# Kernel optimization log

Hardware: AMD Instinct MI355X
Metric: run time of the kernel (lower is better)

## Reference

```python
import jax, jax.numpy as jnp
import numpy as np

N_NODES = 50000
N_EDGES = 800000
DIM_IN, DIM_H, DIM_OUT = 128, 128, 64


def _init_linear(key, fan_in, fan_out):
    # kaiming-uniform-ish init, matches torch Linear scale
    lim = 1.0 / np.sqrt(fan_in)
    return jax.random.uniform(key, (fan_in, fan_out), jnp.float32, -lim, lim)


def setup_inputs() -> dict:
    key = jax.random.key(0)
    ks = jax.random.split(key, 12)
    x = jax.random.normal(ks[0], (N_NODES, DIM_IN), jnp.float32)
    edge_index = jax.random.randint(ks[1], (2, N_EDGES), 0, N_NODES, jnp.int32)
    dims = [(DIM_IN, DIM_H), (DIM_H, DIM_H), (DIM_H, DIM_OUT)]
    inp = {"x": x, "edge_index": edge_index}
    for i, (fi, fo) in enumerate(dims):
        inp[f"Wl{i}"] = _init_linear(ks[2 + 3 * i], fi, fo)   # neighbor transform
        inp[f"Wr{i}"] = _init_linear(ks[3 + 3 * i], fi, fo)   # root transform
        inp[f"b{i}"] = jnp.zeros((fo,), jnp.float32)
    return inp


def _sage_layer(x, src, dst, Wl, Wr, b):
    # mean aggregation of neighbor messages x[src] at destination nodes
    msg = x[src]                                              # [E, d]
    agg = jax.ops.segment_sum(msg, dst, num_segments=N_NODES)  # [N, d]
    cnt = jax.ops.segment_sum(jnp.ones((src.shape[0],), x.dtype), dst,
                              num_segments=N_NODES)
    mean = agg / jnp.maximum(cnt, 1.0)[:, None]               # isolated nodes -> 0
    return mean @ Wl + b + x @ Wr                              # SAGEConv


def reference(x, edge_index, Wl0, Wr0, b0, Wl1, Wr1, b1, Wl2, Wr2, b2):
    src, dst = edge_index[0], edge_index[1]
    layers = [(Wl0, Wr0, b0), (Wl1, Wr1, b1), (Wl2, Wr2, b2)]
    h = x
    for i, (Wl, Wr, b) in enumerate(layers):
        h = _sage_layer(h, src, dst, Wl, Wr, b)
        if i != len(layers) - 1:
            h = jax.nn.relu(h)  # dropout p=0.2 is identity in eval mode
    return jax.nn.log_softmax(h, axis=1), h
```

## Files before the change

kernel.cpp:

```cpp
#include <hip/hip_runtime.h>

#define N_NODES 50000
#define N_EDGES 800000
#define SCAN_BLOCKS 196
#define WIN 6250

typedef __attribute__((ext_vector_type(8))) short short8;
typedef __attribute__((ext_vector_type(4))) float f32x4;
typedef unsigned short ushort_t;
typedef unsigned int uint_t;

__device__ inline ushort_t f2bf(float f) {
    union { float f; uint_t u; } v; v.f = f;
    uint_t u = v.u;
    u += 0x7fffu + ((u >> 16) & 1u);
    return (ushort_t)(u >> 16);
}
__device__ inline float bflo(uint_t v) { return __uint_as_float(v << 16); }
__device__ inline float bfhi(uint_t v) { return __uint_as_float(v & 0xffff0000u); }
__device__ inline float bf2f(ushort_t v) { return __uint_as_float((uint_t)v << 16); }

#define ACC8(V) { a[0] += bflo((V).x); a[1] += bfhi((V).x); \
                  a[2] += bflo((V).y); a[3] += bfhi((V).y); \
                  a[4] += bflo((V).z); a[5] += bfhi((V).z); \
                  a[6] += bflo((V).w); a[7] += bfhi((V).w); }

__global__ void count_edges_mp(const int* __restrict__ ei, int* __restrict__ cnt) {
    int g = blockIdx.x & 7;
    int nb = gridDim.x >> 3;
    int bi = blockIdx.x >> 3;
    int lo = g * WIN;
    for (int e = bi * 256 + threadIdx.x; e < N_EDGES; e += nb * 256) {
        int d = ei[N_EDGES + e];
        if ((unsigned)(d - lo) < WIN) atomicAdd(&cnt[d], 1);
    }
}

__global__ void fill_csr_mp(const int* __restrict__ ei, int* __restrict__ cursor,
                            int* __restrict__ csr_src) {
    int g = blockIdx.x & 7;
    int nb = gridDim.x >> 3;
    int bi = blockIdx.x >> 3;
    int lo = g * WIN;
    for (int e = bi * 256 + threadIdx.x; e < N_EDGES; e += nb * 256) {
        int d = ei[N_EDGES + e];
        if ((unsigned)(d - lo) < WIN) {
            int p = atomicAdd(&cursor[d], 1);
            csr_src[p] = ei[e];
        }
    }
}

__global__ void block_sums(const int* __restrict__ cnt, int* __restrict__ bsum) {
    int i = blockIdx.x * 256 + threadIdx.x;
    int v = (i < N_NODES) ? cnt[i] : 0;
    for (int off = 32; off; off >>= 1) v += __shfl_down(v, off, 64);
    __shared__ int s[4];
    if ((threadIdx.x & 63) == 0) s[threadIdx.x >> 6] = v;
    __syncthreads();
    if (threadIdx.x == 0) bsum[blockIdx.x] = s[0] + s[1] + s[2] + s[3];
}

__global__ void scan_bsums(const int* __restrict__ bsum, int* __restrict__ bprefix,
                           int* __restrict__ rowstart) {
    __shared__ int s[256];
    int t = threadIdx.x;
    int v = (t < SCAN_BLOCKS) ? bsum[t] : 0;
    s[t] = v;
    __syncthreads();
    for (int off = 1; off < 256; off <<= 1) {
        int add = (t >= off) ? s[t - off] : 0;
        __syncthreads();
        s[t] += add;
        __syncthreads();
    }
    bprefix[t] = s[t] - v;
    if (t == 0) rowstart[N_NODES] = N_EDGES;
}

__global__ void apply_scan(const int* __restrict__ cnt, const int* __restrict__ bprefix,
                           int* __restrict__ rowstart, int* __restrict__ cursor) {
    __shared__ int s[256];
    int t = threadIdx.x;
    int i = blockIdx.x * 256 + t;
    int v = (i < N_NODES) ? cnt[i] : 0;
    s[t] = v;
    __syncthreads();
    for (int off = 1; off < 256; off <<= 1) {
        int add = (t >= off) ? s[t - off] : 0;
        __syncthreads();
        s[t] += add;
        __syncthreads();
    }
    int excl = s[t] - v + bprefix[blockIdx.x];
    if (i < N_NODES) { rowstart[i] = excl; cursor[i] = excl; }
}

__global__ void cvt_bf16(const float* __restrict__ in, ushort_t* __restrict__ out, int n4) {
    int i = blockIdx.x * 256 + threadIdx.x;
    if (i < n4) {
        float4 v = ((const float4*)in)[i];
        ushort4 o;
        o.x = f2bf(v.x); o.y = f2bf(v.y); o.z = f2bf(v.z); o.w = f2bf(v.w);
        ((ushort4*)out)[i] = o;
    }
}

__global__ void pack_w256(const float* __restrict__ Wl, const float* __restrict__ Wr,
                          ushort_t* __restrict__ out) {
    int idx = blockIdx.x * 256 + threadIdx.x;
    if (idx >= 8 * 8 * 64 * 8) return;
    int j = idx & 7, l = (idx >> 3) & 63, t = (idx >> 9) & 7, ks = idx >> 12;
    int n = t * 16 + (l & 15);
    int k = ks * 32 + (l >> 4) * 8 + j;
    float w = (k < 128) ? Wl[k * 128 + n] : Wr[(k - 128) * 128 + n];
    out[idx] = f2bf(w);
}

__global__ void pack_wzr(const float* __restrict__ Wl, const float* __restrict__ Wr,
                         ushort_t* __restrict__ out) {
    int idx = blockIdx.x * 256 + threadIdx.x;
    if (idx >= 4 * 8 * 64 * 8) return;
    int j = idx & 7, l = (idx >> 3) & 63, t = (idx >> 9) & 7, ks = idx >> 12;
    int n = t * 16 + (l & 15);
    int k = ks * 32 + (l >> 4) * 8 + j;
    float w = (n < 64) ? Wl[k * 64 + n] : Wr[k * 64 + (n - 64)];
    out[idx] = f2bf(w);
}

__global__ __launch_bounds__(256) void sage_fused(
    const ushort_t* __restrict__ feat_bf,
    const int* __restrict__ rowstart,
    const int* __restrict__ csr_src,
    const ushort_t* __restrict__ Bpk, const float* __restrict__ bias,
    ushort_t* __restrict__ out_bf) {
    __shared__ uint_t mlds[64][68];
    int lane = threadIdx.x & 63;
    int wave = threadIdx.x >> 6;
    int rowBase = blockIdx.x * 64 + wave * 16;
    int sub = lane >> 4;
    int sl  = lane & 15;
    int gb  = sub << 4;
    const uint_t* base = (const uint_t*)feat_bf;

    for (int p = 0; p < 4; ++p) {
        int node = rowBase + p * 4 + sub;
        int s0 = 0, s1 = 0;
        if (node < N_NODES) { s0 = rowstart[node]; s1 = rowstart[node + 1]; }
        float a[8];
        #pragma unroll
        for (int k = 0; k < 8; ++k) a[k] = 0.f;

        int pos = s0;
        while (__any(pos < s1)) {
            int m = min(16, s1 - pos);
            int idxr = (sl < m) ? csr_src[pos + sl] : 0;
            int mm = max(m, 0);
            mm = max(mm, __shfl_xor(mm, 16, 64));
            mm = max(mm, __shfl_xor(mm, 32, 64));
            for (int j = 0; j < mm; j += 8) {
                int  sidx[8];
                bool vld[8];
                #pragma unroll
                for (int k = 0; k < 8; ++k) {
                    int q = __shfl(idxr, (gb + j + k) & 63, 64);
                    vld[k]  = (j + k < m);
                    sidx[k] = vld[k] ? q : 0;
                }
                uint4 V[8];
                #pragma unroll
                for (int k = 0; k < 8; ++k)
                    V[k] = *(const uint4*)(base + (size_t)sidx[k] * 64 + (sl << 2));
                #pragma unroll
                for (int k = 0; k < 8; ++k)
                    if (vld[k]) { ACC8(V[k]); }
            }
            pos += 16;
        }
        float inv = 1.0f / fmaxf((float)(s1 - s0), 1.0f);
        uint4 o;
        o.x = (uint_t)f2bf(a[0] * inv) | ((uint_t)f2bf(a[1] * inv) << 16);
        o.y = (uint_t)f2bf(a[2] * inv) | ((uint_t)f2bf(a[3] * inv) << 16);
        o.z = (uint_t)f2bf(a[4] * inv) | ((uint_t)f2bf(a[5] * inv) << 16);
        o.w = (uint_t)f2bf(a[6] * inv) | ((uint_t)f2bf(a[7] * inv) << 16);
        *((uint4*)&mlds[wave * 16 + p * 4 + sub][sl << 2]) = o;
    }
    __syncthreads();

    int row16 = lane & 15;
    int quad  = lane >> 4;
    int arow  = min(rowBase + row16, N_NODES - 1);
    const ushort_t* rrow = feat_bf + (size_t)arow * 128;
    const short8* bp = (const short8*)Bpk + lane;

    f32x4 acc[8];
    #pragma unroll
    for (int t = 0; t < 8; ++t) { f32x4 z = {0.f, 0.f, 0.f, 0.f}; acc[t] = z; }

    #pragma unroll
    for (int ks = 0; ks < 8; ++ks) {
        short8 afrag;
        if (ks < 4)
            afrag = *(const short8*)&mlds[wave * 16 + row16][ks * 16 + quad * 4];
        else
            afrag = *(const short8*)(rrow + (ks - 4) * 32 + quad * 8);
        #pragma unroll
        for (int t = 0; t < 8; ++t) {
            short8 bfrag = bp[(ks * 8 + t) * 64];
            acc[t] = __builtin_amdgcn_mfma_f32_16x16x32_bf16(afrag, bfrag, acc[t], 0, 0, 0);
        }
    }

    #pragma unroll
    for (int t = 0; t < 8; ++t) {
        int col = t * 16 + row16;
        float bv = bias[col];
        #pragma unroll
        for (int r = 0; r < 4; ++r) {
            int row = rowBase + quad * 4 + r;
            if (row < N_NODES) {
                float v = fmaxf(acc[t][r] + bv, 0.f);
                out_bf[(size_t)row * 128 + col] = f2bf(v);
            }
        }
    }
}

__global__ __launch_bounds__(256) void gemm_zr_pk(
    const ushort_t* __restrict__ h_bf, const ushort_t* __restrict__ Bpk,
    const float* __restrict__ bias,
    ushort_t* __restrict__ z_bf, float* __restrict__ r_f32) {
    int lane = threadIdx.x & 63;
    int wave = threadIdx.x >> 6;
    int row16 = lane & 15;
    int quad = lane >> 4;
    int rowBase = blockIdx.x * 64 + wave * 16;
    int arow = min(rowBase + row16, N_NODES - 1);
    const ushort_t* hrow = h_bf + (size_t)arow * 128;
    const short8* bp = (const short8*)Bpk + lane;

    f32x4 acc[8];
    #pragma unroll
    for (int t = 0; t < 8; ++t) { f32x4 z = {0.f, 0.f, 0.f, 0.f}; acc[t] = z; }

    #pragma unroll
    for (int ks = 0; ks < 4; ++ks) {
        short8 afrag = *(const short8*)(hrow + ks * 32 + quad * 8);
        #pragma unroll
        for (int t = 0; t < 8; ++t) {
            short8 bfrag = bp[(ks * 8 + t) * 64];
            acc[t] = __builtin_amdgcn_mfma_f32_16x16x32_bf16(afrag, bfrag, acc[t], 0, 0, 0);
        }
    }

    #pragma unroll
    for (int t = 0; t < 8; ++t) {
        int col = t * 16 + row16;
        #pragma unroll
        for (int r = 0; r < 4; ++r) {
            int row = rowBase + quad * 4 + r;
            if (row < N_NODES) {
                if (col < 64) {
                    z_bf[(size_t)row * 64 + col] = f2bf(acc[t][r]);
                } else {
                    r_f32[(size_t)row * 64 + (col - 64)] = acc[t][r] + bias[col - 64];
                }
            }
        }
    }
}

__global__ __launch_bounds__(256) void final_agg_softmax2(
    const ushort_t* __restrict__ z_bf, const float* __restrict__ r_f32,
    const int* __restrict__ rowstart, const int* __restrict__ csr_src,
    float* __restrict__ out) {
    int lane = threadIdx.x & 63;
    int wave = threadIdx.x >> 6;
    int sub = lane >> 3;
    int sl  = lane & 7;
    int gb  = sub << 3;
    int node = blockIdx.x * 32 + wave * 8 + sub;
    int s0 = 0, s1 = 0;
    if (node < N_NODES) { s0 = rowstart[node]; s1 = rowstart[node + 1]; }

    float a[8];
    #pragma unroll
    for (int k = 0; k < 8; ++k) a[k] = 0.f;
    const uint_t* zb = (const uint_t*)z_bf;

    int pos = s0;
    while (__any(pos < s1)) {
        int m = min(8, s1 - pos);
        int idxr = (sl < m) ? csr_src[pos + sl] : 0;
        int  sidx[8];
        bool vld[8];
        #pragma unroll
        for (int k = 0; k < 8; ++k) {
            int q = __shfl(idxr, (gb + k) & 63, 64);
            vld[k]  = (k < m);
            sidx[k] = vld[k] ? q : 0;
        }
        uint4 V[8];
        #pragma unroll
        for (int k = 0; k < 8; ++k)
            V[k] = *(const uint4*)(zb + (size_t)sidx[k] * 32 + (sl << 2));
        #pragma unroll
        for (int k = 0; k < 8; ++k)
            if (vld[k]) { ACC8(V[k]); }
        pos += 8;
    }
    if (node >= N_NODES) return;

    float inv = 1.0f / fmaxf((float)(s1 - s0), 1.0f);
    const float4* rr = (const float4*)(r_f32 + (size_t)node * 64 + sl * 8);
    float4 rA = rr[0], rB = rr[1];
    float h[8];
    h[0] = a[0] * inv + rA.x; h[1] = a[1] * inv + rA.y;
    h[2] = a[2] * inv + rA.z; h[3] = a[3] * inv + rA.w;
    h[4] = a[4] * inv + rB.x; h[5] = a[5] * inv + rB.y;
    h[6] = a[6] * inv + rB.z; h[7] = a[7] * inv + rB.w;

    float mx = fmaxf(fmaxf(fmaxf(h[0], h[1]), fmaxf(h[2], h[3])),
                     fmaxf(fmaxf(h[4], h[5]), fmaxf(h[6], h[7])));
    mx = fmaxf(mx, __shfl_xor(mx, 1, 64));
    mx = fmaxf(mx, __shfl_xor(mx, 2, 64));
    mx = fmaxf(mx, __shfl_xor(mx, 4, 64));
    float s = 0.f;
    #pragma unroll
    for (int k = 0; k < 8; ++k) s += expf(h[k] - mx);
    s += __shfl_xor(s, 1, 64);
    s += __shfl_xor(s, 2, 64);
    s += __shfl_xor(s, 4, 64);
    float lse = mx + logf(s);

    size_t o1 = (size_t)node * 64 + sl * 8;
    size_t o2 = (size_t)N_NODES * 64 + o1;
    *(float4*)(out + o1)     = make_float4(h[0] - lse, h[1] - lse, h[2] - lse, h[3] - lse);
    *(float4*)(out + o1 + 4) = make_float4(h[4] - lse, h[5] - lse, h[6] - lse, h[7] - lse);
    *(float4*)(out + o2)     = make_float4(h[0], h[1], h[2], h[3]);
    *(float4*)(out + o2 + 4) = make_float4(h[4], h[5], h[6], h[7]);
}

extern "C" void kernel_launch(void* const* d_in, const int* in_sizes, int n_in,
                              void* d_out, int out_size, void* d_ws, size_t ws_size,
                              hipStream_t stream) {
    const float* x  = (const float*)d_in[0];
    const int* ei   = (const int*)d_in[1];
    const float* Wl0 = (const float*)d_in[2];
    const float* Wr0 = (const float*)d_in[3];
    const float* b0  = (const float*)d_in[4];
    const float* Wl1 = (const float*)d_in[5];
    const float* Wr1 = (const float*)d_in[6];
    const float* b1  = (const float*)d_in[7];
    const float* Wl2 = (const float*)d_in[8];
    const float* Wr2 = (const float*)d_in[9];
    const float* b2  = (const float*)d_in[10];
    float* out = (float*)d_out;

    char* ws = (char*)d_ws;
    int* cnt      = (int*)(ws + 0x000000);
    int* rowstart = (int*)(ws + 0x040000);
    int* cursor   = (int*)(ws + 0x080000);
    int* bsum     = (int*)(ws + 0x0C0000);
    int* bprefix  = (int*)(ws + 0x0C1000);
    int* csr_src  = (int*)(ws + 0x100000);
    ushort_t* pk0 = (ushort_t*)(ws + 0x420000);
    ushort_t* pk1 = (ushort_t*)(ws + 0x440000);
    ushort_t* pkz = (ushort_t*)(ws + 0x460000);
    ushort_t* x_bf  = (ushort_t*)(ws + 0x0500000);
    ushort_t* h_bf  = (ushort_t*)(ws + 0x1200000);
    ushort_t* h2_bf = (ushort_t*)(ws + 0x1F00000);
    ushort_t* z_bf  = (ushort_t*)(ws + 0x0500000);
    float*    r_f32 = (float*)  (ws + 0x1200000);

    pack_w256<<<128, 256, 0, stream>>>(Wl0, Wr0, pk0);
    pack_w256<<<128, 256, 0, stream>>>(Wl1, Wr1, pk1);
    pack_wzr<<<64, 256, 0, stream>>>(Wl2, Wr2, pkz);

    hipMemsetAsync(cnt, 0, N_NODES * sizeof(int), stream);
    count_edges_mp<<<1024, 256, 0, stream>>>(ei, cnt);
    block_sums<<<SCAN_BLOCKS, 256, 0, stream>>>(cnt, bsum);
    scan_bsums<<<1, 256, 0, stream>>>(bsum, bprefix, rowstart);
    apply_scan<<<SCAN_BLOCKS, 256, 0, stream>>>(cnt, bprefix, rowstart, cursor);
    fill_csr_mp<<<1024, 256, 0, stream>>>(ei, cursor, csr_src);

    cvt_bf16<<<6250, 256, 0, stream>>>(x, x_bf, (N_NODES * 128) / 4);

    sage_fused<<<782, 256, 0, stream>>>(x_bf, rowstart, csr_src, pk0, b0, h_bf);

    sage_fused<<<782, 256, 0, stream>>>(h_bf, rowstart, csr_src, pk1, b1, h2_bf);

    gemm_zr_pk<<<782, 256, 0, stream>>>(h2_bf, pkz, b2, z_bf, r_f32);
    final_agg_softmax2<<<1563, 256, 0, stream>>>(z_bf, r_f32, rowstart, csr_src, out);
}
```

Baseline: 297.8 us.

## Split features into 32-dim planes and separate aggregation from GEMM

Stores node features as four 32-column bf16 planes so each aggregation block gathers from a single 3.2MB plane, which is meant to make the random neighbor gathers fit in cache. The fused aggregate+GEMM kernel is split into an aggregation kernel (8 roles per node window, nontemporal index loads and stores) and a GEMM kernel that stages packed weights in LDS. The three weight-pack kernels are merged into one launch. This adds an extra round trip of the mean features through global memory and an additional kernel launch per layer, and reduces the per-lane gather width from 16 bytes to 4 bytes.

```diff
diff --git a/kernel.cpp b/kernel.cpp
--- a/kernel.cpp
+++ b/kernel.cpp
@@ -4,6 +4,7 @@
 #define N_EDGES 800000
 #define SCAN_BLOCKS 196
 #define WIN 6250
+#define PLANE 1600000
 
 typedef __attribute__((ext_vector_type(8))) short short8;
 typedef __attribute__((ext_vector_type(4))) float f32x4;
@@ -96,65 +97,64 @@
     if (i < N_NODES) { rowstart[i] = excl; cursor[i] = excl; }
 }
 
-__global__ void cvt_bf16(const float* __restrict__ in, ushort_t* __restrict__ out, int n4) {
+__global__ void cvt_bf16_pl(const float* __restrict__ in, ushort_t* __restrict__ out) {
     int i = blockIdx.x * 256 + threadIdx.x;
-    if (i < n4) {
-        float4 v = ((const float4*)in)[i];
-        ushort4 o;
-        o.x = f2bf(v.x); o.y = f2bf(v.y); o.z = f2bf(v.z); o.w = f2bf(v.w);
-        ((ushort4*)out)[i] = o;
-    }
-}
-
-__global__ void pack_w256(const float* __restrict__ Wl, const float* __restrict__ Wr,
-                          ushort_t* __restrict__ out) {
-    int idx = blockIdx.x * 256 + threadIdx.x;
-    if (idx >= 8 * 8 * 64 * 8) return;
+    if (i >= 1600000) return;
+    int d0 = (i & 31) * 4;
+    int node = i >> 5;
+    float4 v = ((const float4*)in)[i];
+    ushort4 o;
+    o.x = f2bf(v.x); o.y = f2bf(v.y); o.z = f2bf(v.z); o.w = f2bf(v.w);
+    int p = d0 >> 5, dd = d0 & 31;
+    *(ushort4*)(out + ((size_t)p * 50000 + node) * 32 + dd) = o;
+}
+
+__global__ void pack_all(const float* __restrict__ Wl0, const float* __restrict__ Wr0,
+                         const float* __restrict__ Wl1, const float* __restrict__ Wr1,
+                         const float* __restrict__ Wl2, const float* __restrict__ Wr2,
+                         ushort_t* __restrict__ pk0, ushort_t* __restrict__ pk1,
+                         ushort_t* __restrict__ pkz) {
+    int gi = blockIdx.x * 256 + threadIdx.x;
+    const float* Wl; const float* Wr; ushort_t* dst; int idx; bool zr = false;
+    if (gi < 32768)       { Wl = Wl0; Wr = Wr0; dst = pk0; idx = gi; }
+    else if (gi < 65536)  { Wl = Wl1; Wr = Wr1; dst = pk1; idx = gi - 32768; }
+    else if (gi < 81920)  { Wl = Wl2; Wr = Wr2; dst = pkz; idx = gi - 65536; zr = true; }
+    else return;
     int j = idx & 7, l = (idx >> 3) & 63, t = (idx >> 9) & 7, ks = idx >> 12;
     int n = t * 16 + (l & 15);
     int k = ks * 32 + (l >> 4) * 8 + j;
-    float w = (k < 128) ? Wl[k * 128 + n] : Wr[(k - 128) * 128 + n];
-    out[idx] = f2bf(w);
-}
-
-__global__ void pack_wzr(const float* __restrict__ Wl, const float* __restrict__ Wr,
-                         ushort_t* __restrict__ out) {
-    int idx = blockIdx.x * 256 + threadIdx.x;
-    if (idx >= 4 * 8 * 64 * 8) return;
-    int j = idx & 7, l = (idx >> 3) & 63, t = (idx >> 9) & 7, ks = idx >> 12;
-    int n = t * 16 + (l & 15);
-    int k = ks * 32 + (l >> 4) * 8 + j;
-    float w = (n < 64) ? Wl[k * 64 + n] : Wr[k * 64 + (n - 64)];
-    out[idx] = f2bf(w);
-}
-
-__global__ __launch_bounds__(256) void sage_fused(
-    const ushort_t* __restrict__ feat_bf,
+    float w;
+    if (zr) w = (n < 64) ? Wl[k * 64 + n] : Wr[k * 64 + (n - 64)];
+    else    w = (k < 128) ? Wl[k * 128 + n] : Wr[(k - 128) * 128 + n];
+    dst[idx] = f2bf(w);
+}
+
+__global__ __launch_bounds__(256) void agg_pl(
+    const ushort_t* __restrict__ feat_pl,
     const int* __restrict__ rowstart,
     const int* __restrict__ csr_src,
-    const ushort_t* __restrict__ Bpk, const float* __restrict__ bias,
-    ushort_t* __restrict__ out_bf) {
-    __shared__ uint_t mlds[64][68];
-    int lane = threadIdx.x & 63;
-    int wave = threadIdx.x >> 6;
-    int rowBase = blockIdx.x * 64 + wave * 16;
-    int sub = lane >> 4;
-    int sl  = lane & 15;
-    int gb  = sub << 4;
-    const uint_t* base = (const uint_t*)feat_bf;
+    ushort_t* __restrict__ mean_pl) {
+    int role = blockIdx.x & 7;
+    int wi   = blockIdx.x >> 3;
+    int s    = role >> 1, half = role & 1;
+    int lane = threadIdx.x & 63, wave = threadIdx.x >> 6;
+    int sub = lane >> 4, sl = lane & 15, gb = sub << 4;
+    const uint_t* pbase = (const uint_t*)feat_pl + (size_t)s * (PLANE / 2);
+    uint_t* mbase = (uint_t*)mean_pl + (size_t)s * (PLANE / 2);
+    int nodeBase = half * 25000 + wi * 64 + wave * 16;
+    int nodeLim  = (half + 1) * 25000;
 
     for (int p = 0; p < 4; ++p) {
-        int node = rowBase + p * 4 + sub;
+        int node = nodeBase + p * 4 + sub;
+        bool nv = node < nodeLim;
         int s0 = 0, s1 = 0;
-        if (node < N_NODES) { s0 = rowstart[node]; s1 = rowstart[node + 1]; }
-        float a[8];
-        #pragma unroll
-        for (int k = 0; k < 8; ++k) a[k] = 0.f;
+        if (nv) { s0 = rowstart[node]; s1 = rowstart[node + 1]; }
+        float a0 = 0.f, a1 = 0.f;
 
         int pos = s0;
         while (__any(pos < s1)) {
             int m = min(16, s1 - pos);
-            int idxr = (sl < m) ? csr_src[pos + sl] : 0;
+            int idxr = (sl < m) ? __builtin_nontemporal_load(&csr_src[pos + sl]) : 0;
             int mm = max(m, 0);
             mm = max(mm, __shfl_xor(mm, 16, 64));
             mm = max(mm, __shfl_xor(mm, 32, 64));
@@ -167,85 +167,104 @@
                     vld[k]  = (j + k < m);
                     sidx[k] = vld[k] ? q : 0;
                 }
-                uint4 V[8];
+                uint_t V[8];
                 #pragma unroll
                 for (int k = 0; k < 8; ++k)
-                    V[k] = *(const uint4*)(base + (size_t)sidx[k] * 64 + (sl << 2));
+                    V[k] = pbase[(size_t)sidx[k] * 16 + sl];
                 #pragma unroll
                 for (int k = 0; k < 8; ++k)
-                    if (vld[k]) { ACC8(V[k]); }
+                    if (vld[k]) { a0 += bflo(V[k]); a1 += bfhi(V[k]); }
             }
             pos += 16;
         }
-        float inv = 1.0f / fmaxf((float)(s1 - s0), 1.0f);
-        uint4 o;
-        o.x = (uint_t)f2bf(a[0] * inv) | ((uint_t)f2bf(a[1] * inv) << 16);
-        o.y = (uint_t)f2bf(a[2] * inv) | ((uint_t)f2bf(a[3] * inv) << 16);
-        o.z = (uint_t)f2bf(a[4] * inv) | ((uint_t)f2bf(a[5] * inv) << 16);
-        o.w = (uint_t)f2bf(a[6] * inv) | ((uint_t)f2bf(a[7] * inv) << 16);
-        *((uint4*)&mlds[wave * 16 + p * 4 + sub][sl << 2]) = o;
+        if (nv) {
+            float inv = 1.0f / fmaxf((float)(s1 - s0), 1.0f);
+            uint_t packed = (uint_t)f2bf(a0 * inv) | ((uint_t)f2bf(a1 * inv) << 16);
+            __builtin_nontemporal_store(packed, &mbase[(size_t)node * 16 + sl]);
+        }
+    }
+}
+
+__global__ __launch_bounds__(256) void gemm_pl(
+    const ushort_t* __restrict__ mean_pl, const ushort_t* __restrict__ root_pl,
+    const ushort_t* __restrict__ Bpk, const float* __restrict__ bias,
+    ushort_t* __restrict__ out_pl) {
+    __shared__ ushort_t bsh[32768];
+    {
+        const uint4* src = (const uint4*)Bpk;
+        uint4* dst = (uint4*)bsh;
+        for (int i = threadIdx.x; i < 4096; i += 256) dst[i] = src[i];
     }
     __syncthreads();
 
-    int row16 = lane & 15;
-    int quad  = lane >> 4;
-    int arow  = min(rowBase + row16, N_NODES - 1);
-    const ushort_t* rrow = feat_bf + (size_t)arow * 128;
-    const short8* bp = (const short8*)Bpk + lane;
-
-    f32x4 acc[8];
-    #pragma unroll
-    for (int t = 0; t < 8; ++t) { f32x4 z = {0.f, 0.f, 0.f, 0.f}; acc[t] = z; }
-
-    #pragma unroll
-    for (int ks = 0; ks < 8; ++ks) {
-        short8 afrag;
-        if (ks < 4)
-            afrag = *(const short8*)&mlds[wave * 16 + row16][ks * 16 + quad * 4];
-        else
-            afrag = *(const short8*)(rrow + (ks - 4) * 32 + quad * 8);
-        #pragma unroll
-        for (int t = 0; t < 8; ++t) {
-            short8 bfrag = bp[(ks * 8 + t) * 64];
-            acc[t] = __builtin_amdgcn_mfma_f32_16x16x32_bf16(afrag, bfrag, acc[t], 0, 0, 0);
-        }
-    }
-
-    #pragma unroll
-    for (int t = 0; t < 8; ++t) {
-        int col = t * 16 + row16;
-        float bv = bias[col];
-        #pragma unroll
-        for (int r = 0; r < 4; ++r) {
-            int row = rowBase + quad * 4 + r;
-            if (row < N_NODES) {
-                float v = fmaxf(acc[t][r] + bv, 0.f);
-                out_bf[(size_t)row * 128 + col] = f2bf(v);
-            }
-        }
-    }
-}
-
-__global__ __launch_bounds__(256) void gemm_zr_pk(
-    const ushort_t* __restrict__ h_bf, const ushort_t* __restrict__ Bpk,
-    const float* __restrict__ bias,
-    ushort_t* __restrict__ z_bf, float* __restrict__ r_f32) {
     int lane = threadIdx.x & 63;
     int wave = threadIdx.x >> 6;
     int row16 = lane & 15;
     int quad = lane >> 4;
     int rowBase = blockIdx.x * 64 + wave * 16;
     int arow = min(rowBase + row16, N_NODES - 1);
-    const ushort_t* hrow = h_bf + (size_t)arow * 128;
-    const short8* bp = (const short8*)Bpk + lane;
+    const short8* bp = (const short8*)bsh + lane;
 
     f32x4 acc[8];
     #pragma unroll
     for (int t = 0; t < 8; ++t) { f32x4 z = {0.f, 0.f, 0.f, 0.f}; acc[t] = z; }
 
     #pragma unroll
+    for (int ks = 0; ks < 8; ++ks) {
+        const ushort_t* ab = (ks < 4)
+            ? (mean_pl + ((size_t)ks * 50000 + arow) * 32 + quad * 8)
+            : (root_pl + ((size_t)(ks - 4) * 50000 + arow) * 32 + quad * 8);
+        short8 afrag = *(const short8*)ab;
+        #pragma unroll
+        for (int t = 0; t < 8; ++t) {
+            short8 bfrag = bp[(ks * 8 + t) * 64];
+            acc[t] = __builtin_amdgcn_mfma_f32_16x16x32_bf16(afrag, bfrag, acc[t], 0, 0, 0);
+        }
+    }
+
+    #pragma unroll
+    for (int t = 0; t < 8; ++t) {
+        int col = t * 16 + row16;
+        float bv = bias[col];
+        int pl = col >> 5, dd = col & 31;
+        #pragma unroll
+        for (int r = 0; r < 4; ++r) {
+            int row = rowBase + quad * 4 + r;
+            if (row < N_NODES) {
+                float v = fmaxf(acc[t][r] + bv, 0.f);
+                out_pl[((size_t)pl * 50000 + row) * 32 + dd] = f2bf(v);
+            }
+        }
+    }
+}
+
+__global__ __launch_bounds__(256) void gemm_zr_pl(
+    const ushort_t* __restrict__ h_pl, const ushort_t* __restrict__ Bpk,
+    const float* __restrict__ bias,
+    ushort_t* __restrict__ z_bf, float* __restrict__ r_f32) {
+    __shared__ ushort_t bsh[16384];
+    {
+        const uint4* src = (const uint4*)Bpk;
+        uint4* dst = (uint4*)bsh;
+        for (int i = threadIdx.x; i < 2048; i += 256) dst[i] = src[i];
+    }
+    __syncthreads();
+
+    int lane = threadIdx.x & 63;
+    int wave = threadIdx.x >> 6;
+    int row16 = lane & 15;
+    int quad = lane >> 4;
+    int rowBase = blockIdx.x * 64 + wave * 16;
+    int arow = min(rowBase + row16, N_NODES - 1);
+    const short8* bp = (const short8*)bsh + lane;
+
+    f32x4 acc[8];
+    #pragma unroll
+    for (int t = 0; t < 8; ++t) { f32x4 z = {0.f, 0.f, 0.f, 0.f}; acc[t] = z; }
+
+    #pragma unroll
     for (int ks = 0; ks < 4; ++ks) {
-        short8 afrag = *(const short8*)(hrow + ks * 32 + quad * 8);
+        short8 afrag = *(const short8*)(h_pl + ((size_t)ks * 50000 + arow) * 32 + quad * 8);
         #pragma unroll
         for (int t = 0; t < 8; ++t) {
             short8 bfrag = bp[(ks * 8 + t) * 64];
@@ -367,15 +386,14 @@
     ushort_t* pk0 = (ushort_t*)(ws + 0x420000);
     ushort_t* pk1 = (ushort_t*)(ws + 0x440000);
     ushort_t* pkz = (ushort_t*)(ws + 0x460000);
-    ushort_t* x_bf  = (ushort_t*)(ws + 0x0500000);
-    ushort_t* h_bf  = (ushort_t*)(ws + 0x1200000);
-    ushort_t* h2_bf = (ushort_t*)(ws + 0x1F00000);
-    ushort_t* z_bf  = (ushort_t*)(ws + 0x0500000);
-    float*    r_f32 = (float*)  (ws + 0x1200000);
-
-    pack_w256<<<128, 256, 0, stream>>>(Wl0, Wr0, pk0);
-    pack_w256<<<128, 256, 0, stream>>>(Wl1, Wr1, pk1);
-    pack_wzr<<<64, 256, 0, stream>>>(Wl2, Wr2, pkz);
+    ushort_t* x_pl    = (ushort_t*)(ws + 0x0500000);
+    ushort_t* mean_pl = (ushort_t*)(ws + 0x1200000);
+    ushort_t* h_pl    = (ushort_t*)(ws + 0x1F00000);
+    ushort_t* h2_pl   = (ushort_t*)(ws + 0x2C00000);
+    ushort_t* z_bf    = (ushort_t*)(ws + 0x3900000);
+    float*    r_f32   = (float*)  (ws + 0x4000000);
+
+    pack_all<<<320, 256, 0, stream>>>(Wl0, Wr0, Wl1, Wr1, Wl2, Wr2, pk0, pk1, pkz);
 
     hipMemsetAsync(cnt, 0, N_NODES * sizeof(int), stream);
     count_edges_mp<<<1024, 256, 0, stream>>>(ei, cnt);
@@ -384,12 +402,14 @@
     apply_scan<<<SCAN_BLOCKS, 256, 0, stream>>>(cnt, bprefix, rowstart, cursor);
     fill_csr_mp<<<1024, 256, 0, stream>>>(ei, cursor, csr_src);
 
-    cvt_bf16<<<6250, 256, 0, stream>>>(x, x_bf, (N_NODES * 128) / 4);
-
-    sage_fused<<<782, 256, 0, stream>>>(x_bf, rowstart, csr_src, pk0, b0, h_bf);
-
-    sage_fused<<<782, 256, 0, stream>>>(h_bf, rowstart, csr_src, pk1, b1, h2_bf);
-
-    gemm_zr_pk<<<782, 256, 0, stream>>>(h2_bf, pkz, b2, z_bf, r_f32);
+    cvt_bf16_pl<<<6250, 256, 0, stream>>>(x, x_pl);
+
+    agg_pl<<<3128, 256, 0, stream>>>(x_pl, rowstart, csr_src, mean_pl);
+    gemm_pl<<<782, 256, 0, stream>>>(mean_pl, x_pl, pk0, b0, h_pl);
+
+    agg_pl<<<3128, 256, 0, stream>>>(h_pl, rowstart, csr_src, mean_pl);
+    gemm_pl<<<782, 256, 0, stream>>>(mean_pl, h_pl, pk1, b1, h2_pl);
+
+    gemm_zr_pl<<<782, 256, 0, stream>>>(h2_pl, pkz, b2, z_bf, r_f32);
     final_agg_softmax2<<<1563, 256, 0, stream>>>(z_bf, r_f32, rowstart, csr_src, out);
 }
```

Result: slower. 337.5 us (+13.3%).

## Merge prep kernels and fuse last-layer GEMM into second SAGE layer

Applied to the files above, without the earlier changes.

Merges edge counting, the x to bf16 conversion and the three weight-packing kernels into a single multi-role prep launch. The layer-2 output is staged in LDS and fed straight into the final z/r projection GEMM inside the second fused SAGE kernel, which removes the separate gemm_zr_pk launch and the global write and read of h2. The cost is an extra __syncthreads, LDS reuse, and more register pressure in the fused kernel, and the workspace layout is rearranged so z and r no longer alias x_bf and h_bf.

```diff
diff --git a/kernel.cpp b/kernel.cpp
--- a/kernel.cpp
+++ b/kernel.cpp
@@ -25,14 +25,44 @@
                   a[4] += bflo((V).z); a[5] += bfhi((V).z); \
                   a[6] += bflo((V).w); a[7] += bfhi((V).w); }
 
-__global__ void count_edges_mp(const int* __restrict__ ei, int* __restrict__ cnt) {
-    int g = blockIdx.x & 7;
-    int nb = gridDim.x >> 3;
-    int bi = blockIdx.x >> 3;
-    int lo = g * WIN;
-    for (int e = bi * 256 + threadIdx.x; e < N_EDGES; e += nb * 256) {
-        int d = ei[N_EDGES + e];
-        if ((unsigned)(d - lo) < WIN) atomicAdd(&cnt[d], 1);
+__global__ void prep(const int* __restrict__ ei, int* __restrict__ cnt,
+                     const float* __restrict__ x, ushort_t* __restrict__ x_bf,
+                     const float* __restrict__ Wl0, const float* __restrict__ Wr0,
+                     const float* __restrict__ Wl1, const float* __restrict__ Wr1,
+                     const float* __restrict__ Wl2, const float* __restrict__ Wr2,
+                     ushort_t* __restrict__ pk0, ushort_t* __restrict__ pk1,
+                     ushort_t* __restrict__ pkz) {
+    int b = blockIdx.x;
+    if (b < 1024) {
+        int g = b & 7;
+        int bi = b >> 3;
+        int lo = g * WIN;
+        for (int e = bi * 256 + threadIdx.x; e < N_EDGES; e += 128 * 256) {
+            int d = ei[N_EDGES + e];
+            if ((unsigned)(d - lo) < WIN) atomicAdd(&cnt[d], 1);
+        }
+    } else if (b < 7274) {
+        int i = (b - 1024) * 256 + threadIdx.x;
+        if (i < 1600000) {
+            float4 v = ((const float4*)x)[i];
+            ushort4 o;
+            o.x = f2bf(v.x); o.y = f2bf(v.y); o.z = f2bf(v.z); o.w = f2bf(v.w);
+            ((ushort4*)x_bf)[i] = o;
+        }
+    } else {
+        int gi = (b - 7274) * 256 + threadIdx.x;
+        const float* Wl; const float* Wr; ushort_t* dst; int idx; bool zr = false;
+        if (gi < 32768)       { Wl = Wl0; Wr = Wr0; dst = pk0; idx = gi; }
+        else if (gi < 65536)  { Wl = Wl1; Wr = Wr1; dst = pk1; idx = gi - 32768; }
+        else if (gi < 81920)  { Wl = Wl2; Wr = Wr2; dst = pkz; idx = gi - 65536; zr = true; }
+        else return;
+        int j = idx & 7, l = (idx >> 3) & 63, t = (idx >> 9) & 7, ks = idx >> 12;
+        int n = t * 16 + (l & 15);
+        int k = ks * 32 + (l >> 4) * 8 + j;
+        float w;
+        if (zr) w = (n < 64) ? Wl[k * 64 + n] : Wr[k * 64 + (n - 64)];
+        else    w = (k < 128) ? Wl[k * 128 + n] : Wr[(k - 128) * 128 + n];
+        dst[idx] = f2bf(w);
     }
 }
 
@@ -96,44 +126,15 @@
     if (i < N_NODES) { rowstart[i] = excl; cursor[i] = excl; }
 }
 
-__global__ void cvt_bf16(const float* __restrict__ in, ushort_t* __restrict__ out, int n4) {
-    int i = blockIdx.x * 256 + threadIdx.x;
-    if (i < n4) {
-        float4 v = ((const float4*)in)[i];
-        ushort4 o;
-        o.x = f2bf(v.x); o.y = f2bf(v.y); o.z = f2bf(v.z); o.w = f2bf(v.w);
-        ((ushort4*)out)[i] = o;
-    }
-}
-
-__global__ void pack_w256(const float* __restrict__ Wl, const float* __restrict__ Wr,
-                          ushort_t* __restrict__ out) {
-    int idx = blockIdx.x * 256 + threadIdx.x;
-    if (idx >= 8 * 8 * 64 * 8) return;
-    int j = idx & 7, l = (idx >> 3) & 63, t = (idx >> 9) & 7, ks = idx >> 12;
-    int n = t * 16 + (l & 15);
-    int k = ks * 32 + (l >> 4) * 8 + j;
-    float w = (k < 128) ? Wl[k * 128 + n] : Wr[(k - 128) * 128 + n];
-    out[idx] = f2bf(w);
-}
-
-__global__ void pack_wzr(const float* __restrict__ Wl, const float* __restrict__ Wr,
-                         ushort_t* __restrict__ out) {
-    int idx = blockIdx.x * 256 + threadIdx.x;
-    if (idx >= 4 * 8 * 64 * 8) return;
-    int j = idx & 7, l = (idx >> 3) & 63, t = (idx >> 9) & 7, ks = idx >> 12;
-    int n = t * 16 + (l & 15);
-    int k = ks * 32 + (l >> 4) * 8 + j;
-    float w = (n < 64) ? Wl[k * 64 + n] : Wr[k * 64 + (n - 64)];
-    out[idx] = f2bf(w);
-}
-
-__global__ __launch_bounds__(256) void sage_fused(
+template <bool ZR>
+__global__ __launch_bounds__(256) void sage_fused_k(
     const ushort_t* __restrict__ feat_bf,
     const int* __restrict__ rowstart,
     const int* __restrict__ csr_src,
     const ushort_t* __restrict__ Bpk, const float* __restrict__ bias,
-    ushort_t* __restrict__ out_bf) {
+    const ushort_t* __restrict__ Bz, const float* __restrict__ bias2,
+    ushort_t* __restrict__ out_bf,
+    ushort_t* __restrict__ z_bf, float* __restrict__ r_f32) {
     __shared__ uint_t mlds[64][68];
     int lane = threadIdx.x & 63;
     int wave = threadIdx.x >> 6;
@@ -211,59 +212,61 @@
         }
     }
 
-    #pragma unroll
-    for (int t = 0; t < 8; ++t) {
-        int col = t * 16 + row16;
-        float bv = bias[col];
-        #pragma unroll
-        for (int r = 0; r < 4; ++r) {
-            int row = rowBase + quad * 4 + r;
-            if (row < N_NODES) {
+    if (!ZR) {
+        #pragma unroll
+        for (int t = 0; t < 8; ++t) {
+            int col = t * 16 + row16;
+            float bv = bias[col];
+            #pragma unroll
+            for (int r = 0; r < 4; ++r) {
+                int row = rowBase + quad * 4 + r;
+                if (row < N_NODES) {
+                    float v = fmaxf(acc[t][r] + bv, 0.f);
+                    out_bf[(size_t)row * 128 + col] = f2bf(v);
+                }
+            }
+        }
+    } else {
+        #pragma unroll
+        for (int t = 0; t < 8; ++t) {
+            int col = t * 16 + row16;
+            float bv = bias[col];
+            #pragma unroll
+            for (int r = 0; r < 4; ++r) {
                 float v = fmaxf(acc[t][r] + bv, 0.f);
-                out_bf[(size_t)row * 128 + col] = f2bf(v);
-            }
-        }
-    }
-}
-
-__global__ __launch_bounds__(256) void gemm_zr_pk(
-    const ushort_t* __restrict__ h_bf, const ushort_t* __restrict__ Bpk,
-    const float* __restrict__ bias,
-    ushort_t* __restrict__ z_bf, float* __restrict__ r_f32) {
-    int lane = threadIdx.x & 63;
-    int wave = threadIdx.x >> 6;
-    int row16 = lane & 15;
-    int quad = lane >> 4;
-    int rowBase = blockIdx.x * 64 + wave * 16;
-    int arow = min(rowBase + row16, N_NODES - 1);
-    const ushort_t* hrow = h_bf + (size_t)arow * 128;
-    const short8* bp = (const short8*)Bpk + lane;
-
-    f32x4 acc[8];
-    #pragma unroll
-    for (int t = 0; t < 8; ++t) { f32x4 z = {0.f, 0.f, 0.f, 0.f}; acc[t] = z; }
-
-    #pragma unroll
-    for (int ks = 0; ks < 4; ++ks) {
-        short8 afrag = *(const short8*)(hrow + ks * 32 + quad * 8);
+                ((ushort_t*)&mlds[wave * 16 + quad * 4 + r][0])[col] = f2bf(v);
+            }
+        }
+        __syncthreads();
+
+        const short8* bz = (const short8*)Bz + lane;
+        f32x4 acc2[8];
+        #pragma unroll
+        for (int t = 0; t < 8; ++t) { f32x4 z = {0.f, 0.f, 0.f, 0.f}; acc2[t] = z; }
+
+        #pragma unroll
+        for (int ks = 0; ks < 4; ++ks) {
+            short8 afrag = *(const short8*)((const ushort_t*)&mlds[wave * 16 + row16][0]
+                                            + ks * 32 + quad * 8);
+            #pragma unroll
+            for (int t = 0; t < 8; ++t) {
+                short8 bfrag = bz[(ks * 8 + t) * 64];
+                acc2[t] = __builtin_amdgcn_mfma_f32_16x16x32_bf16(afrag, bfrag, acc2[t], 0, 0, 0);
+            }
+        }
+
         #pragma unroll
         for (int t = 0; t < 8; ++t) {
-            short8 bfrag = bp[(ks * 8 + t) * 64];
-            acc[t] = __builtin_amdgcn_mfma_f32_16x16x32_bf16(afrag, bfrag, acc[t], 0, 0, 0);
-        }
-    }
-
-    #pragma unroll
-    for (int t = 0; t < 8; ++t) {
-        int col = t * 16 + row16;
-        #pragma unroll
-        for (int r = 0; r < 4; ++r) {
-            int row = rowBase + quad * 4 + r;
-            if (row < N_NODES) {
-                if (col < 64) {
-                    z_bf[(size_t)row * 64 + col] = f2bf(acc[t][r]);
-                } else {
-                    r_f32[(size_t)row * 64 + (col - 64)] = acc[t][r] + bias[col - 64];
+            int col = t * 16 + row16;
+            #pragma unroll
+            for (int r = 0; r < 4; ++r) {
+                int row = rowBase + quad * 4 + r;
+                if (row < N_NODES) {
+                    if (col < 64) {
+                        z_bf[(size_t)row * 64 + col] = f2bf(acc2[t][r]);
+                    } else {
+                        r_f32[(size_t)row * 64 + (col - 64)] = acc2[t][r] + bias2[col - 64];
+                    }
                 }
             }
         }
@@ -367,29 +370,25 @@
     ushort_t* pk0 = (ushort_t*)(ws + 0x420000);
     ushort_t* pk1 = (ushort_t*)(ws + 0x440000);
     ushort_t* pkz = (ushort_t*)(ws + 0x460000);
-    ushort_t* x_bf  = (ushort_t*)(ws + 0x0500000);
-    ushort_t* h_bf  = (ushort_t*)(ws + 0x1200000);
-    ushort_t* h2_bf = (ushort_t*)(ws + 0x1F00000);
-    ushort_t* z_bf  = (ushort_t*)(ws + 0x0500000);
-    float*    r_f32 = (float*)  (ws + 0x1200000);
-
-    pack_w256<<<128, 256, 0, stream>>>(Wl0, Wr0, pk0);
-    pack_w256<<<128, 256, 0, stream>>>(Wl1, Wr1, pk1);
-    pack_wzr<<<64, 256, 0, stream>>>(Wl2, Wr2, pkz);
+    ushort_t* x_bf = (ushort_t*)(ws + 0x0500000);
+    ushort_t* h_bf = (ushort_t*)(ws + 0x1200000);
+    ushort_t* z_bf = (ushort_t*)(ws + 0x1F00000);
+    float*    r_f32 = (float*)  (ws + 0x2600000);
 
     hipMemsetAsync(cnt, 0, N_NODES * sizeof(int), stream);
-    count_edges_mp<<<1024, 256, 0, stream>>>(ei, cnt);
+    prep<<<7594, 256, 0, stream>>>(ei, cnt, x, x_bf,
+                                   Wl0, Wr0, Wl1, Wr1, Wl2, Wr2, pk0, pk1, pkz);
+
     block_sums<<<SCAN_BLOCKS, 256, 0, stream>>>(cnt, bsum);
     scan_bsums<<<1, 256, 0, stream>>>(bsum, bprefix, rowstart);
     apply_scan<<<SCAN_BLOCKS, 256, 0, stream>>>(cnt, bprefix, rowstart, cursor);
     fill_csr_mp<<<1024, 256, 0, stream>>>(ei, cursor, csr_src);
 
-    cvt_bf16<<<6250, 256, 0, stream>>>(x, x_bf, (N_NODES * 128) / 4);
-
-    sage_fused<<<782, 256, 0, stream>>>(x_bf, rowstart, csr_src, pk0, b0, h_bf);
-
-    sage_fused<<<782, 256, 0, stream>>>(h_bf, rowstart, csr_src, pk1, b1, h2_bf);
-
-    gemm_zr_pk<<<782, 256, 0, stream>>>(h2_bf, pkz, b2, z_bf, r_f32);
+    sage_fused_k<false><<<782, 256, 0, stream>>>(x_bf, rowstart, csr_src, pk0, b0,
+                                                 nullptr, nullptr, h_bf, nullptr, nullptr);
+
+    sage_fused_k<true><<<782, 256, 0, stream>>>(h_bf, rowstart, csr_src, pk1, b1,
+                                                pkz, b2, nullptr, z_bf, r_f32);
+
     final_agg_softmax2<<<1563, 256, 0, stream>>>(z_bf, r_f32, rowstart, csr_src, out);
 }
```

After: 276.1 us. 1.08x faster.
